# Optimization experiments

Measured on AMD Instinct MI355X. Metric: run time of the kernel, lower is better.

The kernel has to match this reference:

```python
import jax, jax.numpy as jnp
import numpy as np

NUM_HEADS = 16
EPS = 1e-12  # matches torch F.normalize eps


def _l2norm(t):
    n = jnp.sqrt(jnp.sum(t * t, axis=-1, keepdims=True))
    return t / jnp.maximum(n, EPS)


def setup_inputs() -> dict:
    key = jax.random.key(0)
    kx, kq, kk, kv = jax.random.split(key, 4)
    B, S, E = 2, 2048, 1024
    head_dim = E // NUM_HEADS
    bound = 1.0 / np.sqrt(E)  # nn.Linear default init range
    x = jax.random.normal(kx, (B, S, E), dtype=jnp.float32)
    Wq = jax.random.uniform(kq, (E, E), dtype=jnp.float32, minval=-bound, maxval=bound)
    Wk = jax.random.uniform(kk, (E, E), dtype=jnp.float32, minval=-bound, maxval=bound)
    Wv = jax.random.uniform(kv, (E, E), dtype=jnp.float32, minval=-bound, maxval=bound)
    g_scale = jnp.asarray(np.sqrt(head_dim), dtype=jnp.float32)  # 1/d_k = sqrt(head_dim)
    return {"x": x, "Wq": Wq, "Wk": Wk, "Wv": Wv, "g_scale": g_scale}


def reference(x, Wq, Wk, Wv, g_scale):
    B, S, E = x.shape
    H = NUM_HEADS
    D = E // H
    # projections (torch Linear: x @ W.T), split heads -> [B, H, S, D]
    q = (x @ Wq.T).reshape(B, S, H, D).transpose(0, 2, 1, 3)
    k = (x @ Wk.T).reshape(B, S, H, D).transpose(0, 2, 1, 3)
    v = (x @ Wv.T).reshape(B, S, H, D).transpose(0, 2, 1, 3)
    # qk_norm branch: L2-normalize q, k then learnable scale
    q = _l2norm(q)
    k = _l2norm(k)
    scores = g_scale * jnp.einsum('bhqd,bhkd->bhqk', q, k)  # [B, H, S, S]
    attn = jax.nn.softmax(scores, axis=-1)
    # dropout p=0.0 (eval) -> identity
    out = jnp.einsum('bhqk,bhkd->bhqd', attn, v)  # [B, H, S, D]
    out = out.transpose(0, 2, 1, 3).reshape(B, S, E)
    return out
```

## Files before the change

kernel.cpp:

```cpp
#include <hip/hip_runtime.h>
#include <math.h>

#define NH 16
#define HD 64
#define SEQ 2048
#define BAT 2
#define EMB 1024
#define MTOT (BAT*SEQ)
#define NTOT (3*EMB)

typedef __attribute__((ext_vector_type(8))) short bf16x8;
typedef __attribute__((ext_vector_type(4))) float f32x4;

#define MFMA16(a,b,c) __builtin_amdgcn_mfma_f32_16x16x32_bf16(a,b,c,0,0,0)

__device__ inline short f2bf(float f) {
    union { float f; unsigned u; } x; x.f = f;
    unsigned r = (x.u + 0x7FFF + ((x.u >> 16) & 1)) >> 16;
    return (short)r;
}

__device__ inline float fast_exp2(float x) {
#if __has_builtin(__builtin_amdgcn_exp2f)
    return __builtin_amdgcn_exp2f(x);
#else
    float r; asm("v_exp_f32 %0, %1" : "=v"(r) : "v"(x)); return r;
#endif
}

__device__ inline unsigned pack2bf_t(float a, float b) {
    union { float f; unsigned u; } x, y; x.f = a; y.f = b;
    return __builtin_amdgcn_perm(y.u, x.u, 0x07060302u);
}

typedef const __attribute__((address_space(1))) void* gp_t;
typedef __attribute__((address_space(3))) void* lp_t;
__device__ inline void gload16(const void* g, void* l) {
    __builtin_amdgcn_global_load_lds((gp_t)(uintptr_t)g, (lp_t)(uintptr_t)l, 16, 0, 0);
}

#define BARR() asm volatile("s_barrier" ::: "memory")
#define VMW(N) asm volatile("s_waitcnt vmcnt(" #N ")" ::: "memory")

__global__ __launch_bounds__(256) void prep_kernel(
    const float* __restrict__ x, const float* __restrict__ wq,
    const float* __restrict__ wk, const float* __restrict__ wv,
    short* __restrict__ xb, short* __restrict__ wb)
{
    const size_t NX = (size_t)MTOT * EMB;
    const size_t NW = (size_t)EMB * EMB;
    const size_t i4 = ((size_t)blockIdx.x * 256 + threadIdx.x) * 4;
    float4 v; short* dst;
    if (i4 < NX) { v = *(const float4*)(x + i4); dst = xb + i4; }
    else {
        size_t j = i4 - NX;
        const float* s = (j < NW) ? wq : (j < 2 * NW) ? wk : wv;
        v = *(const float4*)(s + (j & (NW - 1)));
        dst = wb + j;
    }
    short4 o; o.x = f2bf(v.x); o.y = f2bf(v.y); o.z = f2bf(v.z); o.w = f2bf(v.w);
    *(short4*)dst = o;
}

__global__ __launch_bounds__(256, 3) void qkv_gemm_fast(
    const short* __restrict__ xb, const short* __restrict__ wb,
    short* __restrict__ qws, short* __restrict__ kws, short* __restrict__ vperm,
    const float* __restrict__ gptr)
{
    __shared__ short smem[3 * 2 * 128 * 32];
    const int m0 = blockIdx.x * 128, n0 = blockIdx.y * 128;
    const int t = threadIdx.x, wave = t >> 6, lane = t & 63;
    const int quad = lane >> 4, l16 = lane & 15;
    const int wm = (wave & 1) * 64, wn = (wave >> 1) * 64;

    const int srow = wave * 32 + (lane >> 2);
    const int scol = ((lane & 3) ^ ((lane >> 3) & 3)) * 8;
    const short* ga = xb + (size_t)(m0 + srow) * EMB + scol;
    const short* gb = wb + (size_t)(n0 + srow) * EMB + scol;

    const int swz = (quad ^ ((l16 >> 1) & 3)) * 8;
    int aoff[4], boff[4];
#pragma unroll
    for (int mf = 0; mf < 4; ++mf) aoff[mf] = (wm + mf * 16 + l16) * 32 + swz;
#pragma unroll
    for (int nf = 0; nf < 4; ++nf) boff[nf] = 4096 + (wn + nf * 16 + l16) * 32 + swz;

    f32x4 acc[4][4] = {};

    auto stageg = [&](int k0, int p) {
        short* lA = smem + p * 8192 + wave * 1024;
        short* lB = smem + p * 8192 + 4096 + wave * 1024;
#pragma unroll
        for (int j = 0; j < 2; ++j) {
            gload16(ga + k0 + (size_t)j * 16 * EMB, lA + j * 512);
            gload16(gb + k0 + (size_t)j * 16 * EMB, lB + j * 512);
        }
    };

    stageg(0, 0);
    stageg(32, 1);
    VMW(4);
    BARR();

    int p = 0, pn = 2;
#pragma unroll 1
    for (int it = 0; it < EMB / 32; ++it) {
        if (it + 2 < EMB / 32) stageg((it + 2) * 32, pn);
        const short* base = smem + p * 8192;
        bf16x8 af[4], bfr[4];
#pragma unroll
        for (int i = 0; i < 4; ++i) af[i]  = *(const bf16x8*)(base + aoff[i]);
#pragma unroll
        for (int i = 0; i < 4; ++i) bfr[i] = *(const bf16x8*)(base + boff[i]);
#pragma unroll
        for (int mf = 0; mf < 4; ++mf)
#pragma unroll
            for (int nf = 0; nf < 4; ++nf)
                acc[mf][nf] = MFMA16(af[mf], bfr[nf], acc[mf][nf]);
        if (it + 2 < EMB / 32) { VMW(4); }
        else                   { VMW(0); }
        BARR();
        p  = (p  == 2) ? 0 : p  + 1;
        pn = (pn == 2) ? 0 : pn + 1;
    }

    short* T = smem;
    const int mat = n0 >> 10;

    if (mat < 2) {
        const float scale = (mat == 0) ? gptr[0] * 1.4426950408889634f : 1.0f;
        float inv[4][4];
#pragma unroll
        for (int mf = 0; mf < 4; ++mf)
#pragma unroll
            for (int reg = 0; reg < 4; ++reg) {
                float ss = 0.f;
#pragma unroll
                for (int nf = 0; nf < 4; ++nf) { float v = acc[mf][nf][reg]; ss += v * v; }
                ss += __shfl_xor(ss, 1, 16);
                ss += __shfl_xor(ss, 2, 16);
                ss += __shfl_xor(ss, 4, 16);
                ss += __shfl_xor(ss, 8, 16);
                inv[mf][reg] = scale / fmaxf(sqrtf(ss), 1e-12f);
            }
#pragma unroll
        for (int mf = 0; mf < 4; ++mf)
#pragma unroll
            for (int nf = 0; nf < 4; ++nf) {
                const int c = wn + nf * 16 + l16;
#pragma unroll
                for (int reg = 0; reg < 4; ++reg) {
                    const int s = wm + mf * 16 + quad * 4 + reg;
                    T[s * 128 + (((c >> 3) ^ (s & 15)) << 3) + (c & 7)] =
                        f2bf(acc[mf][nf][reg] * inv[mf][reg]);
                }
            }
        __syncthreads();
        short* outp = (mat == 0) ? qws : kws;
        const int r = t >> 1, half = t & 1;
        const int sg = m0 + r, bb = sg >> 11, sl = sg & (SEQ - 1);
        const int h = ((n0 & 1023) >> 6) + half;
        short* orow = outp + ((size_t)(bb * NH + h) * SEQ + sl) * HD;
#pragma unroll
        for (int j = 0; j < 8; ++j) {
            int4 v = *(const int4*)&T[r * 128 + ((((half * 8 + j)) ^ (r & 15)) << 3)];
            *(int4*)&orow[j * 8] = v;
        }
    } else {
#pragma unroll
        for (int mf = 0; mf < 4; ++mf)
#pragma unroll
            for (int nf = 0; nf < 4; ++nf) {
                const int c = wn + nf * 16 + l16;
#pragma unroll
                for (int reg = 0; reg < 4; ++reg) {
                    const int s = wm + mf * 16 + quad * 4 + reg;
                    const int sp = (s & ~31) + ((s & 12) >> 2) * 8 + ((s >> 4) & 1) * 4 + (s & 3);
                    T[sp * 128 + (((c >> 3) ^ (sp & 15)) << 3) + (c & 7)] =
                        f2bf(acc[mf][nf][reg]);
                }
            }
        __syncthreads();
        const int c = t >> 1, half = t & 1;
        const int h = ((n0 & 1023) >> 6) + (c >> 6), d = c & 63;
        const int bb = m0 >> 11, p0 = (m0 & (SEQ - 1)) + half * 64;
        short* vrow = vperm + ((size_t)(bb * NH + h) * HD + d) * SEQ + p0;
        const int cg = c >> 3, ce = c & 7;
#pragma unroll
        for (int j = 0; j < 8; ++j) {
            union { int4 v; short s[8]; } tmp;
#pragma unroll
            for (int e = 0; e < 8; ++e) {
                const int s = half * 64 + j * 8 + e;
                tmp.s[e] = T[s * 128 + ((cg ^ (s & 15)) << 3) + ce];
            }
            *(int4*)&vrow[j * 8] = tmp.v;
        }
    }
}

__global__ __launch_bounds__(512, 2) void attn_kernel(
    const short* __restrict__ qws, const short* __restrict__ kws,
    const short* __restrict__ vperm, float* __restrict__ out)
{
    __shared__ short Kt[3][2][2048];
    __shared__ short Vt[3][2][2048];

    const int id = blockIdx.x;
    const int bh = (id & 7) + 8 * (id >> 6);
    const int qt = (id >> 3) & 7;
    const int b = bh >> 4, h = bh & (NH - 1);
    const size_t base = (size_t)bh * SEQ * HD;
    const int t = threadIdx.x, wave = t >> 6, lane = t & 63;
    const int quad = lane >> 4, l16 = lane & 15;

    bf16x8 bq[2][2];
#pragma unroll
    for (int qsub = 0; qsub < 2; ++qsub) {
        const short* qp = qws + base +
            (size_t)(qt * 256 + wave * 32 + qsub * 16 + l16) * HD + quad * 8;
        bq[qsub][0] = *(const bf16x8*)(qp);
        bq[qsub][1] = *(const bf16x8*)(qp + 32);
    }
    bf16x8 ones;
#pragma unroll
    for (int i = 0; i < 8; ++i) ones[i] = (short)0x3F80;

    int koff[4][2];
#pragma unroll
    for (int msub = 0; msub < 4; ++msub)
#pragma unroll
        for (int ks = 0; ks < 2; ++ks)
            koff[msub][ks] = (msub >> 1) * 2048 +
                ((msub & 1) * 16 + l16) * 64 + (((ks * 4 + quad) ^ (l16 & 7)) * 8);
    int voff[4];
#pragma unroll
    for (int nt = 0; nt < 4; ++nt) {
        const int d = nt * 16 + l16;
        voff[nt] = d * 32 + ((quad ^ ((d >> 1) & 3)) * 8);
    }

    f32x4 o_acc[2][4] = {};
    f32x4 l_acc[2] = {};

    auto stage = [&](int tt, int p) {
        if (wave < 4) {
            const int ks = wave >> 1;
#pragma unroll
            for (int j = 0; j < 2; ++j) {
                const int jj = (wave & 1) * 2 + j;
                const int kl = jj * 8 + (lane >> 3);
                const int row = tt * 64 + ks * 32 + kl;
                gload16(kws + base + (size_t)row * HD + (((lane & 7) ^ (kl & 7)) * 8),
                        &Kt[p][ks][jj * 512 + lane * 8]);
            }
        } else {
            const int w = wave - 4, vs = w >> 1;
#pragma unroll
            for (int j = 0; j < 2; ++j) {
                const int jj = (w & 1) * 2 + j;
                const int d = jj * 16 + (lane >> 2);
                const int ug = (lane & 3) ^ ((d >> 1) & 3);
                gload16(vperm + base + (size_t)d * SEQ + tt * 64 + vs * 32 + ug * 8,
                        &Vt[p][vs][jj * 512 + lane * 8]);
            }
        }
    };

    stage(0, 0);
    stage(1, 1);
    VMW(2);
    BARR();

    int p = 0, pn = 2;
#pragma unroll 1
    for (int tt = 0; tt < SEQ / 64; ++tt) {
        if (tt + 2 < SEQ / 64) stage(tt + 2, pn);
        const short* Kp = &Kt[p][0][0];
        const short* Vp = &Vt[p][0][0];

        f32x4 st[4][2];
#pragma unroll
        for (int msub = 0; msub < 4; ++msub) {
            bf16x8 a0 = *(const bf16x8*)(Kp + koff[msub][0]);
            bf16x8 a1 = *(const bf16x8*)(Kp + koff[msub][1]);
#pragma unroll
            for (int qsub = 0; qsub < 2; ++qsub) {
                f32x4 z = {};
                z = MFMA16(a0, bq[qsub][0], z);
                st[msub][qsub] = MFMA16(a1, bq[qsub][1], z);
            }
        }
#pragma unroll
        for (int s = 0; s < 2; ++s) {
            bf16x8 vf[4];
#pragma unroll
            for (int nt = 0; nt < 4; ++nt)
                vf[nt] = *(const bf16x8*)(Vp + s * 2048 + voff[nt]);
#pragma unroll
            for (int qsub = 0; qsub < 2; ++qsub) {
                bf16x8 pa;
                unsigned* pu = (unsigned*)&pa;
                pu[0] = pack2bf_t(fast_exp2(st[2*s][qsub][0]), fast_exp2(st[2*s][qsub][1]));
                pu[1] = pack2bf_t(fast_exp2(st[2*s][qsub][2]), fast_exp2(st[2*s][qsub][3]));
                pu[2] = pack2bf_t(fast_exp2(st[2*s+1][qsub][0]), fast_exp2(st[2*s+1][qsub][1]));
                pu[3] = pack2bf_t(fast_exp2(st[2*s+1][qsub][2]), fast_exp2(st[2*s+1][qsub][3]));
                l_acc[qsub] = MFMA16(pa, ones, l_acc[qsub]);
#pragma unroll
                for (int nt = 0; nt < 4; ++nt)
                    o_acc[qsub][nt] = MFMA16(pa, vf[nt], o_acc[qsub][nt]);
            }
        }
        if (tt + 2 < SEQ / 64) { VMW(2); }
        else                   { VMW(0); }
        BARR();
        p  = (p  == 2) ? 0 : p  + 1;
        pn = (pn == 2) ? 0 : pn + 1;
    }

#pragma unroll
    for (int qsub = 0; qsub < 2; ++qsub) {
        float linv[4];
#pragma unroll
        for (int r = 0; r < 4; ++r)
            linv[r] = 1.0f / l_acc[qsub][r];
        const int s = qt * 256 + wave * 32 + qsub * 16 + quad * 4;
        float* ob = out + ((size_t)b * SEQ + s) * EMB + h * HD + l16;
#pragma unroll
        for (int nt = 0; nt < 4; ++nt)
#pragma unroll
            for (int r = 0; r < 4; ++r)
                ob[(size_t)r * EMB + nt * 16] = o_acc[qsub][nt][r] * linv[r];
    }
}

extern "C" void kernel_launch(void* const* d_in, const int* in_sizes, int n_in,
                              void* d_out, int out_size, void* d_ws, size_t ws_size,
                              hipStream_t stream) {
    (void)in_sizes; (void)n_in; (void)out_size; (void)ws_size;
    const float* x  = (const float*)d_in[0];
    const float* Wq = (const float*)d_in[1];
    const float* Wk = (const float*)d_in[2];
    const float* Wv = (const float*)d_in[3];
    const float* g  = (const float*)d_in[4];
    float* out = (float*)d_out;

    const size_t per = (size_t)BAT * NH * SEQ * HD;
    short* qws   = (short*)d_ws;
    short* kws   = qws + per;
    short* vperm = kws + per;

    short* xb = (short*)out;
    short* wb = xb + (size_t)MTOT * EMB;

    prep_kernel<<<7168, 256, 0, stream>>>(x, Wq, Wk, Wv, xb, wb);
    qkv_gemm_fast<<<dim3(MTOT / 128, NTOT / 128), 256, 0, stream>>>(
        xb, wb, qws, kws, vperm, g);
    attn_kernel<<<(SEQ / 256) * BAT * NH, 512, 0, stream>>>(qws, kws, vperm, out);
}
```

Measured before the change: 156.7 us.

## Fuse fp32-to-bf16 conversion into QKV GEMM loads and drop prep kernel

Removes the separate prep kernel that converted x and the weights to bf16 in global memory. The GEMM now loads fp32 tiles into registers, rounds them to bf16 in-kernel and writes them to LDS, with the load for k+2 overlapping compute on k. This saves a launch and a full write/read round trip of the bf16 copies. In exchange it doubles global read bytes per tile, re-converts each input element once per GEMM block that reads it, raises register pressure, and drops the async global-to-LDS path.

```diff
diff --git a/kernel.cpp b/kernel.cpp
--- a/kernel.cpp
+++ b/kernel.cpp
@@ -20,6 +20,13 @@
     return (short)r;
 }
 
+__device__ inline unsigned pk2(float a, float b) {
+    union { float f; unsigned u; } x, y; x.f = a; y.f = b;
+    unsigned ra = x.u + 0x7FFFu + ((x.u >> 16) & 1u);
+    unsigned rb = y.u + 0x7FFFu + ((y.u >> 16) & 1u);
+    return __builtin_amdgcn_perm(rb, ra, 0x07060302u);
+}
+
 __device__ inline float fast_exp2(float x) {
 #if __has_builtin(__builtin_amdgcn_exp2f)
     return __builtin_amdgcn_exp2f(x);
@@ -41,29 +48,11 @@
 
 #define BARR() asm volatile("s_barrier" ::: "memory")
 #define VMW(N) asm volatile("s_waitcnt vmcnt(" #N ")" ::: "memory")
-
-__global__ __launch_bounds__(256) void prep_kernel(
+#define LGKM0() asm volatile("s_waitcnt lgkmcnt(0)" ::: "memory")
+
+__global__ __launch_bounds__(256, 3) void qkv_gemm_fast(
     const float* __restrict__ x, const float* __restrict__ wq,
     const float* __restrict__ wk, const float* __restrict__ wv,
-    short* __restrict__ xb, short* __restrict__ wb)
-{
-    const size_t NX = (size_t)MTOT * EMB;
-    const size_t NW = (size_t)EMB * EMB;
-    const size_t i4 = ((size_t)blockIdx.x * 256 + threadIdx.x) * 4;
-    float4 v; short* dst;
-    if (i4 < NX) { v = *(const float4*)(x + i4); dst = xb + i4; }
-    else {
-        size_t j = i4 - NX;
-        const float* s = (j < NW) ? wq : (j < 2 * NW) ? wk : wv;
-        v = *(const float4*)(s + (j & (NW - 1)));
-        dst = wb + j;
-    }
-    short4 o; o.x = f2bf(v.x); o.y = f2bf(v.y); o.z = f2bf(v.z); o.w = f2bf(v.w);
-    *(short4*)dst = o;
-}
-
-__global__ __launch_bounds__(256, 3) void qkv_gemm_fast(
-    const short* __restrict__ xb, const short* __restrict__ wb,
     short* __restrict__ qws, short* __restrict__ kws, short* __restrict__ vperm,
     const float* __restrict__ gptr)
 {
@@ -73,10 +62,13 @@
     const int quad = lane >> 4, l16 = lane & 15;
     const int wm = (wave & 1) * 64, wn = (wave >> 1) * 64;
 
-    const int srow = wave * 32 + (lane >> 2);
-    const int scol = ((lane & 3) ^ ((lane >> 3) & 3)) * 8;
-    const short* ga = xb + (size_t)(m0 + srow) * EMB + scol;
-    const short* gb = wb + (size_t)(n0 + srow) * EMB + scol;
+    const int mat = n0 >> 10;
+    const float* wsel = (mat == 0) ? wq : (mat == 1) ? wk : wv;
+
+    const int rl = lane >> 2;
+    const int tg = (lane & 3) ^ ((lane >> 3) & 3);
+    const float* gaf = x    + (size_t)(m0 + wave * 32 + rl) * EMB + tg * 8;
+    const float* gbf = wsel + (size_t)((n0 & 1023) + wave * 32 + rl) * EMB + tg * 8;
 
     const int swz = (quad ^ ((l16 >> 1) & 3)) * 8;
     int aoff[4], boff[4];
@@ -86,26 +78,43 @@
     for (int nf = 0; nf < 4; ++nf) boff[nf] = 4096 + (wn + nf * 16 + l16) * 32 + swz;
 
     f32x4 acc[4][4] = {};
-
-    auto stageg = [&](int k0, int p) {
+    float4 ra[4], rb[4];
+
+    auto loadf = [&](int k0) {
+#pragma unroll
+        for (int j = 0; j < 2; ++j) {
+            ra[j * 2 + 0] = *(const float4*)(gaf + k0 + (size_t)j * 16 * EMB);
+            ra[j * 2 + 1] = *(const float4*)(gaf + k0 + (size_t)j * 16 * EMB + 4);
+            rb[j * 2 + 0] = *(const float4*)(gbf + k0 + (size_t)j * 16 * EMB);
+            rb[j * 2 + 1] = *(const float4*)(gbf + k0 + (size_t)j * 16 * EMB + 4);
+        }
+    };
+    auto cvtwrite = [&](int p) {
         short* lA = smem + p * 8192 + wave * 1024;
         short* lB = smem + p * 8192 + 4096 + wave * 1024;
 #pragma unroll
         for (int j = 0; j < 2; ++j) {
-            gload16(ga + k0 + (size_t)j * 16 * EMB, lA + j * 512);
-            gload16(gb + k0 + (size_t)j * 16 * EMB, lB + j * 512);
+            int4 wA, wB;
+            wA.x = (int)pk2(ra[j*2].x, ra[j*2].y);  wA.y = (int)pk2(ra[j*2].z, ra[j*2].w);
+            wA.z = (int)pk2(ra[j*2+1].x, ra[j*2+1].y); wA.w = (int)pk2(ra[j*2+1].z, ra[j*2+1].w);
+            *(int4*)(lA + j * 512 + lane * 8) = wA;
+            wB.x = (int)pk2(rb[j*2].x, rb[j*2].y);  wB.y = (int)pk2(rb[j*2].z, rb[j*2].w);
+            wB.z = (int)pk2(rb[j*2+1].x, rb[j*2+1].y); wB.w = (int)pk2(rb[j*2+1].z, rb[j*2+1].w);
+            *(int4*)(lB + j * 512 + lane * 8) = wB;
         }
     };
 
-    stageg(0, 0);
-    stageg(32, 1);
-    VMW(4);
+    loadf(0);
+    cvtwrite(0);
+    loadf(32);
+    LGKM0();
     BARR();
 
-    int p = 0, pn = 2;
+    int p = 0;
 #pragma unroll 1
     for (int it = 0; it < EMB / 32; ++it) {
-        if (it + 2 < EMB / 32) stageg((it + 2) * 32, pn);
+        if (it + 1 < EMB / 32) cvtwrite((p == 2) ? 0 : p + 1);
+        if (it + 2 < EMB / 32) loadf((it + 2) * 32);
         const short* base = smem + p * 8192;
         bf16x8 af[4], bfr[4];
 #pragma unroll
@@ -117,15 +126,12 @@
 #pragma unroll
             for (int nf = 0; nf < 4; ++nf)
                 acc[mf][nf] = MFMA16(af[mf], bfr[nf], acc[mf][nf]);
-        if (it + 2 < EMB / 32) { VMW(4); }
-        else                   { VMW(0); }
+        LGKM0();
         BARR();
-        p  = (p  == 2) ? 0 : p  + 1;
-        pn = (pn == 2) ? 0 : pn + 1;
+        p = (p == 2) ? 0 : p + 1;
     }
 
     short* T = smem;
-    const int mat = n0 >> 10;
 
     if (mat < 2) {
         const float scale = (mat == 0) ? gptr[0] * 1.4426950408889634f : 1.0f;
@@ -350,11 +356,7 @@
     short* kws   = qws + per;
     short* vperm = kws + per;
 
-    short* xb = (short*)out;
-    short* wb = xb + (size_t)MTOT * EMB;
-
-    prep_kernel<<<7168, 256, 0, stream>>>(x, Wq, Wk, Wv, xb, wb);
     qkv_gemm_fast<<<dim3(MTOT / 128, NTOT / 128), 256, 0, stream>>>(
-        xb, wb, qws, kws, vperm, g);
+        x, Wq, Wk, Wv, qws, kws, vperm, g);
     attn_kernel<<<(SEQ / 256) * BAT * NH, 512, 0, stream>>>(qws, kws, vperm, out);
 }
```

Result: slower. 161.5 us (+3.1%).
